# Performance work log

Hardware: AMD Instinct MI355X
Metric: run time of the kernel (lower is better)

Reference implementation:

```python
import jax, jax.numpy as jnp
import numpy as np

N = 50000
E = 800000
DESC = 256
IN_CH = DESC + 64  # 320
HEADS = 4
HC = 64  # hidden_channels // heads
HID = HEADS * HC  # 256


def _lin(k, fan_in, fan_out):
    kw, kb = jax.random.split(k)
    s = 1.0 / np.sqrt(fan_in)
    W = jax.random.uniform(kw, (fan_in, fan_out), minval=-s, maxval=s, dtype=jnp.float32)
    b = jax.random.uniform(kb, (fan_out,), minval=-s, maxval=s, dtype=jnp.float32)
    return W, b


def setup_inputs() -> dict:
    key = jax.random.key(0)
    ks = jax.random.split(key, 16)
    x = jax.random.normal(ks[0], (N, DESC), dtype=jnp.float32)
    kpts = jax.random.uniform(ks[1], (N, 2), dtype=jnp.float32) * jnp.array([1216.0, 352.0])
    pts_3d = jax.random.uniform(ks[2], (N, 3), dtype=jnp.float32) * 10.0
    edge_index = jax.random.randint(ks[3], (2, E), 0, N, dtype=jnp.int64)

    W1, b1 = _lin(ks[4], 3, 32)
    W2, b2 = _lin(ks[5], 32, 64)
    Wres, bres = _lin(ks[6], IN_CH, HID)
    Wl, bl = _lin(ks[7], IN_CH, HID)
    Wr, br = _lin(ks[8], IN_CH, HID)
    We, _ = _lin(ks[9], 3, HID)
    att = jax.random.normal(ks[10], (HEADS, HC), dtype=jnp.float32) * 0.1
    conv_bias = jnp.zeros((HID,), dtype=jnp.float32)
    gamma = jnp.ones((HID,), dtype=jnp.float32)
    beta = jnp.zeros((HID,), dtype=jnp.float32)
    Wp, bp = _lin(ks[11], HID, 256)
    return dict(x=x, kpts=kpts, pts_3d=pts_3d, edge_index=edge_index,
                W1=W1, b1=b1, W2=W2, b2=b2, Wres=Wres, bres=bres,
                Wl=Wl, bl=bl, Wr=Wr, br=br, We=We, att=att, conv_bias=conv_bias,
                gamma=gamma, beta=beta, Wp=Wp, bp=bp)


def reference(x, kpts, pts_3d, edge_index, W1, b1, W2, b2, Wres, bres,
              Wl, bl, Wr, br, We, att, conv_bias, gamma, beta, Wp, bp):
    n = x.shape[0]
    norm_uv = kpts / jnp.array([1216.0, 352.0], dtype=kpts.dtype)
    depth = pts_3d[:, 2:3]
    pos_input = jnp.concatenate([norm_uv, depth], axis=-1)  # [N,3]
    pos_feat = jax.nn.silu(pos_input @ W1 + b1) @ W2 + b2   # [N,64]
    node_x = jnp.concatenate([x, pos_feat], axis=-1)        # [N,320]

    src, dst = edge_index[0], edge_index[1]
    rel_uv = norm_uv[dst] - norm_uv[src]                    # [E,2]
    dist = jnp.linalg.norm(rel_uv, axis=-1, keepdims=True)  # [E,1]
    edge_attr = jnp.concatenate([rel_uv, dist], axis=-1)    # [E,3]

    identity = node_x @ Wres + bres                         # [N,256]

    # GATv2Conv (share_weights=False, concat=True, neg_slope=0.2, no self-loops)
    x_l = (node_x @ Wl + bl).reshape(n, HEADS, HC)
    x_r = (node_x @ Wr + br).reshape(n, HEADS, HC)
    e_feat = (edge_attr @ We).reshape(-1, HEADS, HC)        # [E,H,C]

    m = x_l[src] + x_r[dst] + e_feat                        # [E,H,C]
    m = jnp.where(m >= 0, m, 0.2 * m)                       # LeakyReLU(0.2)
    logits = jnp.einsum('ehc,hc->eh', m, att)               # [E,H]

    # segment softmax over incoming edges of each dst node
    lmax = jax.ops.segment_max(logits, dst, num_segments=n)  # [N,H]
    ex = jnp.exp(logits - lmax[dst])
    denom = jax.ops.segment_sum(ex, dst, num_segments=n)     # [N,H]
    alpha = ex / (denom[dst] + 1e-16)                        # [E,H]

    msg = x_l[src] * alpha[:, :, None]                       # [E,H,C]
    out = jax.ops.segment_sum(msg, dst, num_segments=n).reshape(n, HID) + conv_bias

    # LayerNorm
    mu = out.mean(-1, keepdims=True)
    var = out.var(-1, keepdims=True)
    out = (out - mu) / jnp.sqrt(var + 1e-5) * gamma + beta

    out = jax.nn.silu(out)
    out = out + identity
    out = out @ Wp + bp
    return out, alpha
```

## Files before the change

### kernel.cpp

```cpp
#include <hip/hip_runtime.h>
#include <math.h>

#define NN 50000
#define NPAD 50048
#define EE 800000
#define HIDC 256
#define INCH 320

typedef __attribute__((ext_vector_type(8))) short bf16x8;
typedef __attribute__((ext_vector_type(4))) float f32x4;
typedef __attribute__((ext_vector_type(2))) float f32x2;

static __device__ __forceinline__ float4 ld4(const float* p){ return *(const float4*)p; }

static __device__ __forceinline__ unsigned short f2b(float f){
  union { float f; unsigned u; } v; v.f = f;
  unsigned r = v.u + 0x7fffu + ((v.u >> 16) & 1u);
  return (unsigned short)(r >> 16);
}
static __device__ __forceinline__ float b2f(unsigned short u){
  union { unsigned u; float f; } v; v.u = ((unsigned)u) << 16; return v.f;
}
static __device__ __forceinline__ float rlane_f(float v, int l){
  return __uint_as_float(__builtin_amdgcn_readlane(__float_as_uint(v), l));
}
static __device__ __forceinline__ int rlane_i(int v, int l){
  return __builtin_amdgcn_readlane(v, l);
}
static __device__ __forceinline__ f32x2 unpk(unsigned u){
  f32x2 r;
  r.x = __uint_as_float(u << 16);
  r.y = __uint_as_float(u & 0xffff0000u);
  return r;
}
static __device__ __forceinline__ f32x2 fma2(f32x2 a, f32x2 b, f32x2 c){
  return __builtin_elementwise_fma(a, b, c);
}
static __device__ __forceinline__ f32x2 max2(f32x2 a, f32x2 b){
  return __builtin_elementwise_max(a, b);
}
static __device__ __forceinline__ f32x2 set2(float v){ f32x2 r; r.x = v; r.y = v; return r; }

typedef const __attribute__((address_space(1))) unsigned int* gas_u32;
typedef __attribute__((address_space(3))) unsigned int* las_u32;
static __device__ __forceinline__ void gload_lds16(const void* g, void* l){
  __builtin_amdgcn_global_load_lds((gas_u32)g, (las_u32)l, 16, 0, 0);
}

__global__ void cvt_x_kernel(const float* __restrict__ x, unsigned short* __restrict__ nodex)
{
  int t = blockIdx.x*blockDim.x + threadIdx.x;
  int row = t >> 6;
  if (row >= NN) return;
  int c4 = (t & 63) * 4;
  float4 v = ld4(x + (size_t)row*256 + c4);
  ushort4 o;
  o.x = f2b(v.x); o.y = f2b(v.y); o.z = f2b(v.z); o.w = f2b(v.w);
  *(ushort4*)(nodex + (size_t)row*320 + c4) = o;
}

__global__ void node_mlp_kernel(const float* __restrict__ kpts,
                                const float* __restrict__ pts3d,
                                const float* __restrict__ W1, const float* __restrict__ b1,
                                const float* __restrict__ W2, const float* __restrict__ b2,
                                unsigned short* __restrict__ nodex,
                                float* __restrict__ nuv)
{
  int i = blockIdx.x*blockDim.x + threadIdx.x;
  if (i >= NN) return;
  float u = kpts[2*i]   * (1.0f/1216.0f);
  float v = kpts[2*i+1] * (1.0f/352.0f);
  float d = pts3d[3*i+2];
  float2 uv; uv.x = u; uv.y = v;
  *(float2*)(nuv + 2*i) = uv;
  float h[32];
#pragma unroll
  for (int j=0;j<32;++j){
    float t = u*W1[j] + v*W1[32+j] + d*W1[64+j] + b1[j];
    h[j] = t / (1.0f + __expf(-t));
  }
  for (int o=0;o<64;o+=4){
    float s0=b2[o], s1=b2[o+1], s2=b2[o+2], s3=b2[o+3];
#pragma unroll
    for (int j=0;j<32;++j){
      float hj = h[j];
      const float* w = W2 + j*64 + o;
      s0 += hj*w[0]; s1 += hj*w[1]; s2 += hj*w[2]; s3 += hj*w[3];
    }
    ushort4 r; r.x=f2b(s0); r.y=f2b(s1); r.z=f2b(s2); r.w=f2b(s3);
    *(ushort4*)(nodex + (size_t)i*320 + 256 + o) = r;
  }
}

__global__ void cvt_w_kernel(const float* __restrict__ Wres, const float* __restrict__ Wl,
                             const float* __restrict__ Wr,   const float* __restrict__ Wp,
                             const float* __restrict__ bres, const float* __restrict__ bl,
                             const float* __restrict__ br,
                             unsigned short* __restrict__ wt, float* __restrict__ biascat)
{
  int t = blockIdx.x*blockDim.x + threadIdx.x;
  if (t < 245760) {
    int which = t / 81920;
    int rem = t % 81920;
    int n = rem / 320, k = rem % 320;
    const float* W = (which == 0) ? Wres : (which == 1) ? Wl : Wr;
    wt[(size_t)which*81920 + rem] = f2b(W[(size_t)k*256 + n]);
  } else if (t < 311296) {
    int r = t - 245760;
    int n = r / 256, k = r % 256;
    wt[245760 + r] = f2b(Wp[(size_t)k*256 + n]);
  } else {
    int r = t - 311296;
    const float* src = (r < 256) ? bres : (r < 512) ? bl : br;
    biascat[r] = src[r & 255];
  }
}

#define GK 64
__global__ __launch_bounds__(256) void mfma_gemm_kernel(
    const unsigned short* __restrict__ A,
    const unsigned short* __restrict__ BT,
    const float* __restrict__ bias,
    float* __restrict__ Cf,
    unsigned short* __restrict__ Cx1,
    unsigned short* __restrict__ Cx2,
    int M, int K, int npan, int ncols)
{
  __shared__ unsigned short Als[128*GK];
  __shared__ unsigned short Bls[128*GK];
  int tid = threadIdx.x;
  int lane = tid & 63, wave = tid >> 6;
  int wm = (wave >> 1) * 64, wn = (wave & 1) * 64;

  int bid = blockIdx.x;
  int fullp = (npan >> 3) << 3;
  int nfull = fullp * ncols;
  int p, c;
  if (bid < nfull) {
    int g  = bid / (8*ncols);
    int r  = bid - g*(8*ncols);
    c  = r >> 3;
    p  = g*8 + (r & 7);
  } else {
    int r = bid - nfull;
    int tail = npan - fullp;
    p = fullp + r % tail;
    c = r / tail;
  }
  int row0 = p * 128, col0 = c * 128;

  f32x4 acc[4][4];
#pragma unroll
  for (int i=0;i<4;++i)
#pragma unroll
    for (int j=0;j<4;++j){ acc[i][j].x=0.f; acc[i][j].y=0.f; acc[i][j].z=0.f; acc[i][j].w=0.f; }

  int fm = lane & 15;
  int q4 = lane >> 4;

  for (int k0 = 0; k0 < K; k0 += GK) {
#pragma unroll
    for (int it = 0; it < 4; ++it) {
      int cgl = it*256 + tid;
      int r = cgl >> 3;
      int kb = ((cgl ^ r) & 7) * 8;
      gload_lds16(A  + (size_t)(row0 + r)*K + k0 + kb, Als + (it*256 + wave*64)*8);
      gload_lds16(BT + (size_t)(col0 + r)*K + k0 + kb, Bls + (it*256 + wave*64)*8);
    }
    __syncthreads();

#pragma unroll
    for (int kk = 0; kk < 2; ++kk) {
      int j = kk*4 + q4;
      bf16x8 af[4], bfr[4];
#pragma unroll
      for (int mi=0; mi<4; ++mi){
        int row = wm + mi*16 + fm;
        af[mi] = *(const bf16x8*)&Als[row*GK + ((j ^ row) & 7)*8];
      }
#pragma unroll
      for (int ni=0; ni<4; ++ni){
        int row = wn + ni*16 + fm;
        bfr[ni] = *(const bf16x8*)&Bls[row*GK + ((j ^ row) & 7)*8];
      }
#pragma unroll
      for (int mi=0; mi<4; ++mi)
#pragma unroll
        for (int ni=0; ni<4; ++ni)
          acc[mi][ni] = __builtin_amdgcn_mfma_f32_16x16x32_bf16(af[mi], bfr[ni], acc[mi][ni], 0, 0, 0);
    }
    __syncthreads();
  }

  int seg = col0 >> 8;
  int colbase = col0 - seg*256;
  int cn = lane & 15, cr = (lane >> 4) * 4;
#pragma unroll
  for (int ni=0; ni<4; ++ni){
    int gcol = col0 + wn + ni*16 + cn;
    int col  = colbase + wn + ni*16 + cn;
    float bb = bias[gcol];
#pragma unroll
    for (int mi=0; mi<4; ++mi){
#pragma unroll
      for (int r=0; r<4; ++r){
        int row = row0 + wm + mi*16 + cr + r;
        if (row < M){
          float v = acc[mi][ni][r] + bb;
          if (seg == 0)      Cf [(size_t)row*256 + col] = v;
          else if (seg == 1) Cx1[(size_t)row*256 + col] = f2b(v);
          else               Cx2[(size_t)row*256 + col] = f2b(v);
        }
      }
    }
  }
}

__global__ void hist_kernel(const int* __restrict__ ei, int* __restrict__ deg){
  int e = blockIdx.x*blockDim.x + threadIdx.x;
  if (e < EE) atomicAdd(&deg[ei[EE + e]], 1);
}

__global__ __launch_bounds__(1024) void scan1_kernel(const int* __restrict__ deg,
                                                     int* __restrict__ incl, int* __restrict__ bsum){
  __shared__ int wsums[16];
  int t = threadIdx.x, lane = t & 63, w = t >> 6;
  int i = blockIdx.x*1024 + t;
  int v = (i < NN) ? deg[i] : 0;
  int sc = v;
#pragma unroll
  for (int off = 1; off < 64; off <<= 1) {
    int o = __shfl_up(sc, off, 64);
    if (lane >= off) sc += o;
  }
  if (lane == 63) wsums[w] = sc;
  __syncthreads();
  if (w == 0) {
    int ws = (lane < 16) ? wsums[lane] : 0;
#pragma unroll
    for (int off = 1; off < 16; off <<= 1) {
      int o = __shfl_up(ws, off, 64);
      if (lane >= off) ws += o;
    }
    if (lane < 16) wsums[lane] = ws;
  }
  __syncthreads();
  int woff = (w > 0) ? wsums[w-1] : 0;
  if (i < NN) incl[i] = sc + woff;
  if (t == 1023) bsum[blockIdx.x] = woff + sc;
}

__global__ void scan2_kernel(int* __restrict__ bsum, int nblk){
  int lane = threadIdx.x;
  int v = (lane < nblk) ? bsum[lane] : 0;
#pragma unroll
  for (int off = 1; off < 64; off <<= 1) {
    int o = __shfl_up(v, off, 64);
    if (lane >= off) v += o;
  }
  if (lane < nblk) bsum[lane] = v;
}

__global__ __launch_bounds__(1024) void scan3_kernel(const int* __restrict__ incl,
                                                     const int* __restrict__ deg,
                                                     const int* __restrict__ bsum,
                                                     int* __restrict__ rowptr, int* __restrict__ cursor,
                                                     int nblk){
  int i = blockIdx.x*1024 + threadIdx.x;
  if (i < NN) {
    int b = blockIdx.x;
    int prev = (b > 0) ? bsum[b-1] : 0;
    int ex = prev + incl[i] - deg[i];
    rowptr[i] = ex;
    cursor[i] = ex;
  }
  if (i == 0) rowptr[NN] = bsum[nblk-1];
}

__global__ void scatter_kernel(const int* __restrict__ ei,
                               int* __restrict__ cursor,
                               uint2* __restrict__ sedata){
  int e = blockIdx.x*blockDim.x + threadIdx.x;
  if (e >= EE) return;
  int s = ei[e];
  int d = ei[EE + e];
  int pos = atomicAdd(&cursor[d], 1);
  uint2 se; se.x = (unsigned)s; se.y = (unsigned)e;
  sedata[pos] = se;
}

#define LOAD8(Q, B0)                                               \
  if ((B0) < cnt) {                                                \
    _Pragma("unroll")                                              \
    for (int t = 0; t < 8; ++t) {                                  \
      int sj = rlane_i(s, ((B0) + t) & 63);                        \
      Q[t] = *(const uint2*)(xlp + ((size_t)sj << 8));             \
    }                                                              \
  }

#define PROC8(Q, B0)                                               \
  _Pragma("unroll")                                                \
  for (int t = 0; t < 8; ++t) {                                    \
    int j = (B0) + t;                                              \
    if (j < cnt) {                                                 \
      float ruj = rlane_f(edx, j);                                 \
      float rvj = rlane_f(edy, j);                                 \
      float dj  = rlane_f(edz, j);                                 \
      f32x2 x01 = unpk(Q[t].x), x23 = unpk(Q[t].y);                \
      f32x2 t01 = fma2(set2(ruj), we0a, xr01);                     \
      t01 = fma2(set2(rvj), we1a, t01);                            \
      t01 = fma2(set2(dj),  we2a, t01);                            \
      t01 = t01 + x01;                                             \
      f32x2 t23 = fma2(set2(ruj), we0b, xr23);                     \
      t23 = fma2(set2(rvj), we1b, t23);                            \
      t23 = fma2(set2(dj),  we2b, t23);                            \
      t23 = t23 + x23;                                             \
      t01 = max2(t01, t01*0.2f);                                   \
      t23 = max2(t23, t23*0.2f);                                   \
      f32x2 pd = t01*atta;                                         \
      pd = fma2(t23, attb, pd);                                    \
      float p = pd.x + pd.y;                                       \
      p += __shfl_xor(p, 1, 64);                                   \
      p += __shfl_xor(p, 2, 64);                                   \
      p += __shfl_xor(p, 4, 64);                                   \
      p += __shfl_xor(p, 8, 64);                                   \
      float exv = __expf(p);                                       \
      denom += exv;                                                \
      int ej = rlane_i(e, j);                                      \
      if ((lane & 15) == 0) alpha_out[(size_t)ej*4 + head] = exv;  \
      f32x2 ex2 = set2(exv);                                       \
      agg01 = fma2(ex2, x01, agg01);                               \
      agg23 = fma2(ex2, x23, agg23);                               \
    }                                                              \
  }

__global__ __launch_bounds__(128) void node_attn_kernel(
    const uint2* __restrict__ sedata, const float* __restrict__ nuv,
    const unsigned short* __restrict__ xl, const unsigned short* __restrict__ xr,
    const float* __restrict__ We, const float* __restrict__ att,
    const float* __restrict__ cbias, const float* __restrict__ gamma,
    const float* __restrict__ beta,
    const int* __restrict__ rowptr,
    const float* __restrict__ identity,
    float* __restrict__ alpha_out, float* __restrict__ denom_buf,
    unsigned short* __restrict__ hbuf)
{
  int wid  = threadIdx.x >> 6;
  int lane = threadIdx.x & 63;
  int v = blockIdx.x*2 + wid;
  if (v >= NN) return;
  int c0 = lane*4;
  int head = lane >> 4;

  f32x2 we0a, we0b, we1a, we1b, we2a, we2b, atta, attb;
  we0a.x = We[c0];       we0a.y = We[c0+1];       we0b.x = We[c0+2];       we0b.y = We[c0+3];
  we1a.x = We[256+c0];   we1a.y = We[256+c0+1];   we1b.x = We[256+c0+2];   we1b.y = We[256+c0+3];
  we2a.x = We[512+c0];   we2a.y = We[512+c0+1];   we2b.x = We[512+c0+2];   we2b.y = We[512+c0+3];
  atta.x = att[c0];      atta.y = att[c0+1];      attb.x = att[c0+2];      attb.y = att[c0+3];
  uint2 xrq = *(const uint2*)(xr + (size_t)v*256 + c0);
  f32x2 xr01 = unpk(xrq.x), xr23 = unpk(xrq.y);
  const unsigned short* xlp = xl + c0;
  float2 duv = *(const float2*)(nuv + 2*(size_t)v);

  int rs = rowptr[v], re = rowptr[v+1];
  int deg = re - rs;

  float denom = 0.f;
  f32x2 agg01 = set2(0.f), agg23 = set2(0.f);

  for (int base = 0; base < deg; base += 64) {
    int cnt = min(64, deg - base);
    int s = 0, e = 0;
    if (lane < cnt) {
      uint2 se = sedata[rs + base + lane];
      s = (int)se.x;
      e = (int)se.y;
    }
    float2 suv = *(const float2*)(nuv + 2*(size_t)s);
    float edx = duv.x - suv.x;
    float edy = duv.y - suv.y;
    float edz = sqrtf(edx*edx + edy*edy);

    uint2 qa[8], qb[8];
    LOAD8(qa, 0);
    for (int b0 = 0; b0 < cnt; b0 += 16) {
      LOAD8(qb, b0 + 8);
      PROC8(qa, b0);
      LOAD8(qa, b0 + 16);
      PROC8(qb, b0 + 8);
    }
  }

  float rdenom = 1.0f / (denom + 1e-16f);
  if ((lane & 15) == 0) denom_buf[(size_t)v*4 + head] = denom;

  float a0 = agg01.x*rdenom + cbias[c0];
  float a1 = agg01.y*rdenom + cbias[c0+1];
  float a2 = agg23.x*rdenom + cbias[c0+2];
  float a3 = agg23.y*rdenom + cbias[c0+3];

  float ps  = a0 + a1 + a2 + a3;
  float ps2 = a0*a0 + a1*a1 + a2*a2 + a3*a3;
#pragma unroll
  for (int off = 1; off < 64; off <<= 1) {
    ps  += __shfl_xor(ps,  off, 64);
    ps2 += __shfl_xor(ps2, off, 64);
  }
  float mu  = ps  * (1.0f/256.0f);
  float var = ps2 * (1.0f/256.0f) - mu*mu;
  float rstd = rsqrtf(var + 1e-5f);
  float4 g  = ld4(gamma + c0);
  float4 b  = ld4(beta  + c0);
  float4 idv = ld4(identity + (size_t)v*256 + c0);
  float y0 = (a0 - mu)*rstd*g.x + b.x;
  float y1 = (a1 - mu)*rstd*g.y + b.y;
  float y2 = (a2 - mu)*rstd*g.z + b.z;
  float y3 = (a3 - mu)*rstd*g.w + b.w;
  y0 = y0 / (1.0f + __expf(-y0)) + idv.x;
  y1 = y1 / (1.0f + __expf(-y1)) + idv.y;
  y2 = y2 / (1.0f + __expf(-y2)) + idv.z;
  y3 = y3 / (1.0f + __expf(-y3)) + idv.w;
  ushort4 hq; hq.x=f2b(y0); hq.y=f2b(y1); hq.z=f2b(y2); hq.w=f2b(y3);
  *(ushort4*)(hbuf + (size_t)v*256 + c0) = hq;
}

__global__ void alpha_fin_kernel(const int* __restrict__ ei, const float* __restrict__ denom_buf,
                                 float* __restrict__ alpha)
{
  int e = blockIdx.x*blockDim.x + threadIdx.x;
  if (e >= EE) return;
  int d = ei[EE + e];
  float4 dn = ld4(denom_buf + (size_t)d*4);
  float4 a = ld4(alpha + (size_t)e*4);
  a.x /= (dn.x + 1e-16f);
  a.y /= (dn.y + 1e-16f);
  a.z /= (dn.z + 1e-16f);
  a.w /= (dn.w + 1e-16f);
  *(float4*)(alpha + (size_t)e*4) = a;
}

extern "C" void kernel_launch(void* const* d_in, const int* in_sizes, int n_in,
                              void* d_out, int out_size, void* d_ws, size_t ws_size,
                              hipStream_t stream)
{
  const float* x      = (const float*)d_in[0];
  const float* kpts   = (const float*)d_in[1];
  const float* pts3d  = (const float*)d_in[2];
  const int*   ei     = (const int*)d_in[3];
  const float* W1     = (const float*)d_in[4];
  const float* b1     = (const float*)d_in[5];
  const float* W2     = (const float*)d_in[6];
  const float* b2     = (const float*)d_in[7];
  const float* Wres   = (const float*)d_in[8];
  const float* bres   = (const float*)d_in[9];
  const float* Wl     = (const float*)d_in[10];
  const float* bl     = (const float*)d_in[11];
  const float* Wr     = (const float*)d_in[12];
  const float* br     = (const float*)d_in[13];
  const float* We     = (const float*)d_in[14];
  const float* att    = (const float*)d_in[15];
  const float* cbias  = (const float*)d_in[16];
  const float* gamma  = (const float*)d_in[17];
  const float* beta   = (const float*)d_in[18];
  const float* Wp     = (const float*)d_in[19];
  const float* bp     = (const float*)d_in[20];

  float* out       = (float*)d_out;
  float* alpha_out = out + (size_t)NN*HIDC;

  float* wsf = (float*)d_ws;
  float*          identity = wsf;
  unsigned short* xl       = (unsigned short*)(wsf + 12800000);
  unsigned short* xr       = (unsigned short*)(wsf + 19206144);
  unsigned short* nodex    = (unsigned short*)(wsf + 25612288);
  unsigned short* hbuf     = (unsigned short*)(wsf + 25612288);
  unsigned short* wt       = (unsigned short*)(wsf + 33619968);
  float*          biascat  = wsf + 33775616;
  float*          denomb   = wsf + 33776384;
  uint2*          sedata   = (uint2*)(wsf + 33976384);
  float*          nuv      = wsf + 35576384;
  int*            incl     = (int*)(wsf + 37176384);
  int*            deg      = (int*)(wsf + 37976384);
  int*            rowptr   = (int*)(wsf + 38026384);
  int*            cursor   = (int*)(wsf + 38076385);
  int*            bsum     = (int*)(wsf + 38126385);

  unsigned short* wtcat = wt;
  unsigned short* wtp   = wt + 245760;

  cvt_x_kernel<<<12500, 256, 0, stream>>>(x, nodex);
  node_mlp_kernel<<<(NN+255)/256, 256, 0, stream>>>(kpts, pts3d, W1, b1, W2, b2, nodex, nuv);
  cvt_w_kernel<<<1219, 256, 0, stream>>>(Wres, Wl, Wr, Wp, bres, bl, br, wt, biascat);

  mfma_gemm_kernel<<<391*6, 256, 0, stream>>>(nodex, wtcat, biascat, identity, xl, xr,
                                              NN, INCH, NPAD/128, 6);

  hipMemsetAsync(deg, 0, NN*sizeof(int), stream);
  hist_kernel<<<(EE+255)/256, 256, 0, stream>>>(ei, deg);
  int nblk = (NN + 1023) / 1024;
  scan1_kernel<<<nblk, 1024, 0, stream>>>(deg, incl, bsum);
  scan2_kernel<<<1, 64, 0, stream>>>(bsum, nblk);
  scan3_kernel<<<nblk, 1024, 0, stream>>>(incl, deg, bsum, rowptr, cursor, nblk);
  scatter_kernel<<<(EE+255)/256, 256, 0, stream>>>(ei, cursor, sedata);

  node_attn_kernel<<<(NN+1)/2, 128, 0, stream>>>(sedata, nuv, xl, xr, We, att,
                                                 cbias, gamma, beta,
                                                 rowptr, identity,
                                                 alpha_out, denomb, hbuf);
  alpha_fin_kernel<<<(EE+255)/256, 256, 0, stream>>>(ei, denomb, alpha_out);

  mfma_gemm_kernel<<<391*2, 256, 0, stream>>>(hbuf, wtp, bp, out, nullptr, nullptr,
                                              NN, HIDC, NPAD/128, 2);
}
```

Before: 538.7 us.

## Double-buffer GEMM LDS tiles with halved K-step to overlap loads and MFMA

Converts the bf16 MFMA GEMM main loop from a single LDS buffer with K-step 64 to two LDS buffers with K-step 32. The next tile's global-to-LDS loads are issued before computing on the current tile, and the swizzle is adapted to 4 chunks per row. This aims to hide global load latency behind MFMA work and drops one barrier per step. In exchange it doubles the number of loop iterations, and the second barrier that guarded buffer reuse is gone, which relies on the async LDS loads being complete when the remaining barrier is reached.

After: 540.7 us. About the same (+0.4%).

```diff
diff --git a/kernel.cpp b/kernel.cpp
--- a/kernel.cpp
+++ b/kernel.cpp
@@ -116,7 +116,7 @@
   }
 }
 
-#define GK 64
+#define GK 32
 __global__ __launch_bounds__(256) void mfma_gemm_kernel(
     const unsigned short* __restrict__ A,
     const unsigned short* __restrict__ BT,
@@ -126,8 +126,8 @@
     unsigned short* __restrict__ Cx2,
     int M, int K, int npan, int ncols)
 {
-  __shared__ unsigned short Als[128*GK];
-  __shared__ unsigned short Bls[128*GK];
+  __shared__ unsigned short Als[2][128*GK];
+  __shared__ unsigned short Bls[2][128*GK];
   int tid = threadIdx.x;
   int lane = tid & 63, wave = tid >> 6;
   int wm = (wave >> 1) * 64, wn = (wave & 1) * 64;
@@ -158,39 +158,50 @@
   int fm = lane & 15;
   int q4 = lane >> 4;
 
-  for (int k0 = 0; k0 < K; k0 += GK) {
-#pragma unroll
-    for (int it = 0; it < 4; ++it) {
-      int cgl = it*256 + tid;
-      int r = cgl >> 3;
-      int kb = ((cgl ^ r) & 7) * 8;
-      gload_lds16(A  + (size_t)(row0 + r)*K + k0 + kb, Als + (it*256 + wave*64)*8);
-      gload_lds16(BT + (size_t)(col0 + r)*K + k0 + kb, Bls + (it*256 + wave*64)*8);
-    }
+#define STAGE_T(d, kk0)                                                      \
+  {                                                                          \
+    _Pragma("unroll")                                                        \
+    for (int it = 0; it < 2; ++it) {                                         \
+      int cgl = it*256 + tid;                                                \
+      int r = cgl >> 2;                                                      \
+      int sc = (cgl ^ r) & 3;                                                \
+      gload_lds16(A  + (size_t)(row0 + r)*K + (kk0) + sc*8,                  \
+                  Als[d] + (it*256 + wave*64)*8);                            \
+      gload_lds16(BT + (size_t)(col0 + r)*K + (kk0) + sc*8,                  \
+                  Bls[d] + (it*256 + wave*64)*8);                            \
+    }                                                                        \
+  }
+
+  int nsteps = K / GK;
+  STAGE_T(0, 0);
+  __syncthreads();
+  int cur = 0;
+  for (int s = 0; s < nsteps; ++s) {
+    if (s + 1 < nsteps) STAGE_T(cur ^ 1, (s + 1) * GK);
+
+    const unsigned short* ab = Als[cur];
+    const unsigned short* bb = Bls[cur];
+    bf16x8 af[4], bfr[4];
+#pragma unroll
+    for (int mi=0; mi<4; ++mi){
+      int row = wm + mi*16 + fm;
+      af[mi] = *(const bf16x8*)&ab[(row*4 + ((q4 ^ row) & 3))*8];
+    }
+#pragma unroll
+    for (int ni=0; ni<4; ++ni){
+      int row = wn + ni*16 + fm;
+      bfr[ni] = *(const bf16x8*)&bb[(row*4 + ((q4 ^ row) & 3))*8];
+    }
+#pragma unroll
+    for (int mi=0; mi<4; ++mi)
+#pragma unroll
+      for (int ni=0; ni<4; ++ni)
+        acc[mi][ni] = __builtin_amdgcn_mfma_f32_16x16x32_bf16(af[mi], bfr[ni], acc[mi][ni], 0, 0, 0);
+
     __syncthreads();
-
-#pragma unroll
-    for (int kk = 0; kk < 2; ++kk) {
-      int j = kk*4 + q4;
-      bf16x8 af[4], bfr[4];
-#pragma unroll
-      for (int mi=0; mi<4; ++mi){
-        int row = wm + mi*16 + fm;
-        af[mi] = *(const bf16x8*)&Als[row*GK + ((j ^ row) & 7)*8];
-      }
-#pragma unroll
-      for (int ni=0; ni<4; ++ni){
-        int row = wn + ni*16 + fm;
-        bfr[ni] = *(const bf16x8*)&Bls[row*GK + ((j ^ row) & 7)*8];
-      }
-#pragma unroll
-      for (int mi=0; mi<4; ++mi)
-#pragma unroll
-        for (int ni=0; ni<4; ++ni)
-          acc[mi][ni] = __builtin_amdgcn_mfma_f32_16x16x32_bf16(af[mi], bfr[ni], acc[mi][ni], 0, 0, 0);
-    }
-    __syncthreads();
-  }
+    cur ^= 1;
+  }
+#undef STAGE_T
 
   int seg = col0 >> 8;
   int colbase = col0 - seg*256;
```
